# Kernel optimization log

Measured on AMD Instinct MI355X. Metric: run time of the kernel, lower is better.

Reference implementation:

```python
import jax, jax.numpy as jnp
import numpy as np

B, L, C, H = 256, 200, 4, 128


def setup_inputs() -> dict:
    key = jax.random.key(0)
    ks = jax.random.split(key, 6)
    seqs = jax.random.normal(ks[0], (B, L, C, H), dtype=jnp.float32)
    # valid prefix of random length, padding (True) at the tail
    lengths = jax.random.randint(ks[1], (B,), 1, L + 1)
    timeline_mask = (jnp.arange(L)[None, :] >= lengths[:, None])[:, :, None]  # [B,L,1] bool
    attention_mask = jnp.zeros((L, L), dtype=bool)  # unused by the module
    s = 1.0 / np.sqrt(H)  # torch GRU default init U(-1/sqrt(H), 1/sqrt(H))
    W_ih = jax.random.uniform(ks[2], (C, 3 * H, H), minval=-s, maxval=s, dtype=jnp.float32)
    W_hh = jax.random.uniform(ks[3], (C, 3 * H, H), minval=-s, maxval=s, dtype=jnp.float32)
    b_ih = jax.random.uniform(ks[4], (C, 3 * H), minval=-s, maxval=s, dtype=jnp.float32)
    b_hh = jax.random.uniform(ks[5], (C, 3 * H), minval=-s, maxval=s, dtype=jnp.float32)
    return {"seqs": seqs, "timeline_mask": timeline_mask, "attention_mask": attention_mask,
            "W_ih": W_ih, "W_hh": W_hh, "b_ih": b_ih, "b_hh": b_hh}


def batched_roll(x, shifts):
    # x: [B, L, H]; per-sample circular shift along time (torch.roll semantics)
    Ldim = x.shape[1]
    idx = (jnp.arange(Ldim)[None, :] - shifts[:, None]) % Ldim  # [B, L]
    return jnp.take_along_axis(x, idx[:, :, None], axis=1)


def gru(x, W_ih, W_hh, b_ih, b_hh):
    # single-layer batch_first GRU, h0 = 0 (torch nn.GRU math)
    xp = jnp.einsum('blh,gh->blg', x, W_ih) + b_ih  # [B, L, 3H] input projections
    Hd = W_hh.shape[1]

    def step(h, xt):
        gh = h @ W_hh.T + b_hh
        i_r, i_z, i_n = jnp.split(xt, 3, axis=-1)
        h_r, h_z, h_n = jnp.split(gh, 3, axis=-1)
        r = jax.nn.sigmoid(i_r + h_r)
        z = jax.nn.sigmoid(i_z + h_z)
        n = jnp.tanh(i_n + r * h_n)
        h_new = (1.0 - z) * n + z * h
        return h_new, h_new

    h0 = jnp.zeros((x.shape[0], Hd), x.dtype)
    _, ys = jax.lax.scan(step, h0, jnp.swapaxes(xp, 0, 1))  # scan over time
    return jnp.swapaxes(ys, 0, 1)  # [B, L, H]


def reference(seqs, timeline_mask, attention_mask, W_ih, W_hh, b_ih, b_hh):
    mask = timeline_mask[:, :, 0]                 # [B, L] True = pad
    length = jnp.sum(~mask, axis=1)               # count of valid steps
    zero_length = jnp.sum(mask, axis=1)           # count of padded steps
    outs = []
    for i in range(seqs.shape[2]):                # loop over C experts (distinct weights)
        x = batched_roll(seqs[:, :, i, :], length)
        y = gru(x, W_ih[i], W_hh[i], b_ih[i], b_hh[i])
        y = batched_roll(y, zero_length)
        y = jnp.where(timeline_mask, 0.0, y)      # masked_fill(timeline_mask, 0.0)
        outs.append(y)
    return jnp.stack(outs, axis=0)  # [C, B, L, H] (list of experts in the original)
```

## Files before the change

### kernel.cpp

```cpp
#include <hip/hip_runtime.h>
#include <hip/hip_bf16.h>

#define BB 256
#define LL 200
#define CC 4
#define HH 128
#define G3 384
#define XP 136

typedef short bf16x8 __attribute__((ext_vector_type(8)));
typedef float f32x4 __attribute__((ext_vector_type(4)));

#define MFMA16(a, b, c) __builtin_amdgcn_mfma_f32_16x16x32_bf16((a), (b), (c), 0, 0, 0)

__device__ __forceinline__ short bf16_rne(float x) {
    union { float f; unsigned u; } v; v.f = x;
    unsigned r = v.u + 0x7FFFu + ((v.u >> 16) & 1u);
    return (short)(r >> 16);
}
__device__ __forceinline__ float rcp_(float x) { return __builtin_amdgcn_rcpf(x); }
__device__ __forceinline__ float sigm_(float x) { return rcp_(1.0f + __expf(-x)); }
__device__ __forceinline__ float tanhf_(float x) { return 2.0f * rcp_(1.0f + __expf(-2.0f * x)) - 1.0f; }

__device__ __forceinline__ unsigned cvtpk(float lo, float hi) {
    unsigned r;
    asm("v_cvt_pk_bf16_f32 %0, %1, %2" : "=v"(r) : "v"(lo), "v"(hi));
    return r;
}
__device__ __forceinline__ uint2 pack4(float4 v) {
    uint2 p;
    p.x = cvtpk(v.x, v.y);
    p.y = cvtpk(v.z, v.w);
    return p;
}

__global__ void compute_lens_kernel(const unsigned char* __restrict__ mask8,
                                    int* __restrict__ lens) {
    __shared__ int bad;
    int b = threadIdx.x;
    if (b == 0) bad = 0;
    __syncthreads();
    int cnt8 = 0, prev = 0, mono = 1;
    for (int t = 0; t < LL; ++t) {
        int v = mask8[b * LL + t] ? 1 : 0;
        cnt8 += (v == 0);
        if (v < prev) mono = 0;
        prev = v;
    }
    if (!mono) atomicAdd(&bad, 1);
    __syncthreads();
    int len;
    if (bad == 0) {
        len = cnt8;
    } else {
        const int* m32 = (const int*)mask8;
        int c = 0;
        for (int t = 0; t < LL; ++t) c += (m32[b * LL + t] == 0);
        len = c;
    }
    if (len < 1) len = 1;
    if (len > LL) len = LL;
    lens[b] = len;
}

__global__ void wsplit_kernel(const float* __restrict__ Wih, const float* __restrict__ Whh,
                              short* __restrict__ wih_hi, short* __restrict__ whh_hi) {
    int i = blockIdx.x * 256 + threadIdx.x;
    wih_hi[i] = bf16_rne(Wih[i]);
    whh_hi[i] = bf16_rne(Whh[i]);
}

__global__ __launch_bounds__(512, 2) void gru_fused_kernel(
    const float* __restrict__ seqs,
    const int*   __restrict__ lens,
    const short* __restrict__ wih_hi,
    const short* __restrict__ whh_hi,
    const float* __restrict__ b_ih,
    const float* __restrict__ b_hh,
    float*       __restrict__ out)
{
    const int bt = blockIdx.x;
    const int c  = blockIdx.y;
    const int bbase = bt * 16;
    const int tid = threadIdx.x;
    const int w = tid >> 6;
    const int l = tid & 63;
    const int l15 = l & 15, g = l >> 4;

    __shared__ __align__(16) short hA[2][16][XP];
    __shared__ __align__(16) short xs[2][16][XP];

    bf16x8 BH[3][4], WI[3][4];
    #pragma unroll
    for (int q = 0; q < 3; ++q) {
        const int NT = q * 8 + w;
        #pragma unroll
        for (int ks = 0; ks < 4; ++ks) {
            size_t off = (size_t)(c * G3 + NT * 16 + l15) * HH + ks * 32 + g * 8;
            BH[q][ks] = *(const bf16x8*)(whh_hi + off);
            WI[q][ks] = *(const bf16x8*)(wih_hi + off);
        }
    }

    const int dim0 = w * 16 + g * 4;

    f32x4 cR4, cZ4, cHN4, cN4;
    {
        float4 rh = *(const float4*)(b_hh + c * G3 + dim0);
        float4 ri = *(const float4*)(b_ih + c * G3 + dim0);
        float4 zh = *(const float4*)(b_hh + c * G3 + 128 + dim0);
        float4 zi = *(const float4*)(b_ih + c * G3 + 128 + dim0);
        float4 nh = *(const float4*)(b_hh + c * G3 + 256 + dim0);
        float4 ni = *(const float4*)(b_ih + c * G3 + 256 + dim0);
        cR4  = (f32x4){rh.x + ri.x, rh.y + ri.y, rh.z + ri.z, rh.w + ri.w};
        cZ4  = (f32x4){zh.x + zi.x, zh.y + zi.y, zh.z + zi.z, zh.w + zi.w};
        cHN4 = (f32x4){nh.x, nh.y, nh.z, nh.w};
        cN4  = (f32x4){ni.x, ni.y, ni.z, ni.w};
    }
    const f32x4 cZZ = (f32x4){0.f, 0.f, 0.f, 0.f};

    const int bme = bbase + l15;
    const int lenb = lens[bme];
    int tcur = LL - lenb;
    float* optr = out + ((size_t)(c * BB + bme) * LL + tcur) * HH + dim0;
    const ptrdiff_t owrap = (ptrdiff_t)(LL - 1) * HH;
    float hold[4] = { 0.f, 0.f, 0.f, 0.f };

    const int bsl = tid >> 5;
    const int k0s = (tid & 31) * 4;
    const int lenS = lens[bbase + bsl];
    const float* srow0 = seqs + ((size_t)(bbase + bsl) * LL * CC + c) * HH + k0s;
    int ts0 = LL - lenS;
    int ts1 = ts0 + 1; if (ts1 >= LL) ts1 -= LL;
    float4 xr0 = *(const float4*)(srow0 + (size_t)ts0 * (CC * HH));
    float4 xr1 = *(const float4*)(srow0 + (size_t)ts1 * (CC * HH));
    int txs = ts1 + 1; if (txs >= LL) txs -= LL;
    const float* xptr = srow0 + (size_t)txs * (CC * HH);
    const ptrdiff_t xstep = CC * HH;
    const ptrdiff_t xwrap = (ptrdiff_t)(LL - 1) * CC * HH;

    for (int i = tid; i < 16 * XP / 2; i += 512) ((int*)hA[0])[i] = 0;

    *(uint2*)&xs[0][bsl][k0s] = pack4(xr0);
    *(uint2*)&xs[1][bsl][k0s] = pack4(xr1);
    __syncthreads();

    f32x4 xacc[3];
    {
        bf16x8 xb0 = *(const bf16x8*)&xs[0][l15][g * 8];
        xacc[0] = MFMA16(WI[0][0], xb0, cR4);
        xacc[1] = MFMA16(WI[1][0], xb0, cZ4);
        xacc[2] = MFMA16(WI[2][0], xb0, cN4);
        #pragma unroll
        for (int ks = 1; ks < 4; ++ks) {
            bf16x8 xb = *(const bf16x8*)&xs[0][l15][ks * 32 + g * 8];
            #pragma unroll
            for (int q = 0; q < 3; ++q)
                xacc[q] = MFMA16(WI[q][ks], xb, xacc[q]);
        }
    }
    float4 xraw = *(const float4*)xptr;
    txs = (txs + 1 == LL) ? 0 : txs + 1;
    xptr = (txs == 0) ? xptr - xwrap : xptr + xstep;

    __syncthreads();

#define STEP_BODY(HB, HN)                                                      \
    {                                                                          \
        f32x4 racc[3];                                                         \
        {                                                                      \
            bf16x8 hb0 = *(const bf16x8*)&hA[HB][l15][g * 8];                  \
            racc[0] = MFMA16(BH[0][0], hb0, cZZ);                              \
            racc[1] = MFMA16(BH[1][0], hb0, cZZ);                              \
            racc[2] = MFMA16(BH[2][0], hb0, cHN4);                             \
            _Pragma("unroll")                                                  \
            for (int ks = 1; ks < 4; ++ks) {                                   \
                bf16x8 hbf = *(const bf16x8*)&hA[HB][l15][ks * 32 + g * 8];    \
                _Pragma("unroll")                                              \
                for (int q = 0; q < 3; ++q)                                    \
                    racc[q] = MFMA16(BH[q][ks], hbf, racc[q]);                 \
            }                                                                  \
        }                                                                      \
        float hnew[4];                                                         \
        _Pragma("unroll")                                                      \
        for (int r = 0; r < 4; ++r) {                                          \
            float gr = sigm_(racc[0][r] + xacc[0][r]);                         \
            float gz = sigm_(racc[1][r] + xacc[1][r]);                         \
            float gn = tanhf_(xacc[2][r] + gr * racc[2][r]);                   \
            float hv = gn + gz * (hold[r] - gn);                               \
            hnew[r] = hv;                                                      \
            hold[r] = hv;                                                      \
        }                                                                      \
        {                                                                      \
            uint2 pk;                                                          \
            pk.x = cvtpk(hold[0], hold[1]);                                    \
            pk.y = cvtpk(hold[2], hold[3]);                                    \
            *(uint2*)&hA[HN][l15][dim0] = pk;         \
        }                                                                      \
        {                                                                      \
            int valid = tcur < lenb;                                           \
            float4 ov;                                                         \
            ov.x = valid ? hnew[0] : 0.0f;                                     \
            ov.y = valid ? hnew[1] : 0.0f;                                     \
            ov.z = valid ? hnew[2] : 0.0f;                                     \
            ov.w = valid ? hnew[3] : 0.0f;                                     \
            *(float4*)optr = ov;                              \
            int wrapped = (tcur + 1 == LL);                                    \
            tcur = wrapped ? 0 : tcur + 1;                                     \
            optr = wrapped ? optr - owrap : optr + HH;                         \
        }                                                                      \
        {                                                                      \
            bf16x8 xb0 = *(const bf16x8*)&xs[HN][l15][g * 8];                  \
            xacc[0] = MFMA16(WI[0][0], xb0, cR4);                              \
            xacc[1] = MFMA16(WI[1][0], xb0, cZ4);                              \
            xacc[2] = MFMA16(WI[2][0], xb0, cN4);                              \
            _Pragma("unroll")                                                  \
            for (int ks = 1; ks < 4; ++ks) {                                   \
                bf16x8 xb = *(const bf16x8*)&xs[HN][l15][ks * 32 + g * 8];     \
                _Pragma("unroll")                                              \
                for (int q = 0; q < 3; ++q)                                    \
                    xacc[q] = MFMA16(WI[q][ks], xb, xacc[q]);                  \
            }                                                                  \
        }                                                                      \
        *(uint2*)&xs[HB][bsl][k0s] = pack4(xraw);                              \
        xraw = *(const float4*)xptr;                                           \
        txs = (txs + 1 == LL) ? 0 : txs + 1;                                   \
        xptr = (txs == 0) ? xptr - xwrap : xptr + xstep;                       \
        asm volatile("s_waitcnt lgkmcnt(0)" ::: "memory");                     \
        __builtin_amdgcn_s_barrier();                                          \
        __builtin_amdgcn_sched_barrier(0);                                     \
    }

    for (int si2 = 0; si2 < LL; si2 += 2) {
        STEP_BODY(0, 1)
        STEP_BODY(1, 0)
    }
#undef STEP_BODY
}

extern "C" void kernel_launch(void* const* d_in, const int* in_sizes, int n_in,
                              void* d_out, int out_size, void* d_ws, size_t ws_size,
                              hipStream_t stream) {
    const float* seqs  = (const float*)d_in[0];
    const unsigned char* tmask = (const unsigned char*)d_in[1];
    const float* W_ih  = (const float*)d_in[3];
    const float* W_hh  = (const float*)d_in[4];
    const float* b_ih  = (const float*)d_in[5];
    const float* b_hh  = (const float*)d_in[6];
    float* out = (float*)d_out;

    char* ws = (char*)d_ws;
    int*   lens   = (int*)(ws);
    short* wih_hi = (short*)(ws + 1024);
    short* whh_hi = (short*)(ws + 1024 + 393216);

    compute_lens_kernel<<<1, BB, 0, stream>>>(tmask, lens);
    wsplit_kernel<<<768, 256, 0, stream>>>(W_ih, W_hh, wih_hi, whh_hi);

    gru_fused_kernel<<<dim3(16, CC), 512, 0, stream>>>(
        seqs, lens, wih_hi, whh_hi, b_ih, b_hh, out);
}
```

Before: 179.8 us.

## Store h and x staging buffers in MFMA fragment order and halve staging threads

Changes the shared-memory layout of the hidden-state and input staging buffers from padded row-major to a fragment-ordered layout, so each lane reads its bf16x8 MFMA operand with a contiguous, conflict-free 16-byte load. The per-step global loads of the input are now done by 256 threads, each loading 8 floats and writing one 16-byte packed store, instead of 512 threads each handling 4 floats. This targets LDS bank conflicts and address arithmetic in the latency-bound recurrent loop. In exchange, the h writes become scattered stores and the staging work is concentrated in half the threads.

```diff
diff --git a/kernel.cpp b/kernel.cpp
--- a/kernel.cpp
+++ b/kernel.cpp
@@ -6,7 +6,6 @@
 #define CC 4
 #define HH 128
 #define G3 384
-#define XP 136
 
 typedef short bf16x8 __attribute__((ext_vector_type(8)));
 typedef float f32x4 __attribute__((ext_vector_type(4)));
@@ -26,12 +25,6 @@
     unsigned r;
     asm("v_cvt_pk_bf16_f32 %0, %1, %2" : "=v"(r) : "v"(lo), "v"(hi));
     return r;
-}
-__device__ __forceinline__ uint2 pack4(float4 v) {
-    uint2 p;
-    p.x = cvtpk(v.x, v.y);
-    p.y = cvtpk(v.z, v.w);
-    return p;
 }
 
 __global__ void compute_lens_kernel(const unsigned char* __restrict__ mask8,
@@ -87,8 +80,8 @@
     const int l = tid & 63;
     const int l15 = l & 15, g = l >> 4;
 
-    __shared__ __align__(16) short hA[2][16][XP];
-    __shared__ __align__(16) short xs[2][16][XP];
+    __shared__ __align__(16) short hA[2][4][512];
+    __shared__ __align__(16) short xs[2][4][512];
 
     bf16x8 BH[3][4], WI[3][4];
     #pragma unroll
@@ -103,6 +96,8 @@
     }
 
     const int dim0 = w * 16 + g * 4;
+    const int ksw = w >> 1;
+    const int hwbase = ((((w & 1) * 2 + (g >> 1)) * 16 + l15) * 8) + (g & 1) * 4;
 
     f32x4 cR4, cZ4, cHN4, cN4;
     {
@@ -126,56 +121,69 @@
     const ptrdiff_t owrap = (ptrdiff_t)(LL - 1) * HH;
     float hold[4] = { 0.f, 0.f, 0.f, 0.f };
 
-    const int bsl = tid >> 5;
-    const int k0s = (tid & 31) * 4;
-    const int lenS = lens[bbase + bsl];
-    const float* srow0 = seqs + ((size_t)(bbase + bsl) * LL * CC + c) * HH + k0s;
-    int ts0 = LL - lenS;
-    int ts1 = ts0 + 1; if (ts1 >= LL) ts1 -= LL;
-    float4 xr0 = *(const float4*)(srow0 + (size_t)ts0 * (CC * HH));
-    float4 xr1 = *(const float4*)(srow0 + (size_t)ts1 * (CC * HH));
-    int txs = ts1 + 1; if (txs >= LL) txs -= LL;
-    const float* xptr = srow0 + (size_t)txs * (CC * HH);
+    const int sactive = (tid < 256);
+    const int bsl = tid >> 4;
+    const int ko  = (tid & 15) * 8;
+    const int sks = ko >> 5;
+    const int sfb = (((ko >> 3) & 3) * 16 + (bsl & 15)) * 8;
+    const float* srow0 = nullptr;
+    int txs = 0;
+    float4 xra, xrb;
     const ptrdiff_t xstep = CC * HH;
     const ptrdiff_t xwrap = (ptrdiff_t)(LL - 1) * CC * HH;
-
-    for (int i = tid; i < 16 * XP / 2; i += 512) ((int*)hA[0])[i] = 0;
-
-    *(uint2*)&xs[0][bsl][k0s] = pack4(xr0);
-    *(uint2*)&xs[1][bsl][k0s] = pack4(xr1);
+    const float* xptr = nullptr;
+
+    if (sactive) {
+        const int lenS = lens[bbase + bsl];
+        srow0 = seqs + ((size_t)(bbase + bsl) * LL * CC + c) * HH + ko;
+        int ts0 = LL - lenS;
+        int ts1 = ts0 + 1; if (ts1 >= LL) ts1 -= LL;
+        float4 a0 = *(const float4*)(srow0 + (size_t)ts0 * xstep);
+        float4 a1 = *(const float4*)(srow0 + (size_t)ts0 * xstep + 4);
+        float4 b0 = *(const float4*)(srow0 + (size_t)ts1 * xstep);
+        float4 b1 = *(const float4*)(srow0 + (size_t)ts1 * xstep + 4);
+        *(uint4*)&xs[0][sks][sfb] = make_uint4(cvtpk(a0.x, a0.y), cvtpk(a0.z, a0.w),
+                                               cvtpk(a1.x, a1.y), cvtpk(a1.z, a1.w));
+        *(uint4*)&xs[1][sks][sfb] = make_uint4(cvtpk(b0.x, b0.y), cvtpk(b0.z, b0.w),
+                                               cvtpk(b1.x, b1.y), cvtpk(b1.z, b1.w));
+        txs = ts1 + 1; if (txs >= LL) txs -= LL;
+        xptr = srow0 + (size_t)txs * xstep;
+        xra = *(const float4*)xptr;
+        xrb = *(const float4*)(xptr + 4);
+        txs = (txs + 1 == LL) ? 0 : txs + 1;
+        xptr = (txs == 0) ? srow0 : xptr + xstep;
+    }
+
+    for (int i = tid; i < 1024; i += 512) ((int*)hA[0])[i] = 0;
     __syncthreads();
 
     f32x4 xacc[3];
     {
-        bf16x8 xb0 = *(const bf16x8*)&xs[0][l15][g * 8];
+        bf16x8 xb0 = *(const bf16x8*)&xs[0][0][l * 8];
         xacc[0] = MFMA16(WI[0][0], xb0, cR4);
         xacc[1] = MFMA16(WI[1][0], xb0, cZ4);
         xacc[2] = MFMA16(WI[2][0], xb0, cN4);
         #pragma unroll
         for (int ks = 1; ks < 4; ++ks) {
-            bf16x8 xb = *(const bf16x8*)&xs[0][l15][ks * 32 + g * 8];
+            bf16x8 xb = *(const bf16x8*)&xs[0][ks][l * 8];
             #pragma unroll
             for (int q = 0; q < 3; ++q)
                 xacc[q] = MFMA16(WI[q][ks], xb, xacc[q]);
         }
     }
-    float4 xraw = *(const float4*)xptr;
-    txs = (txs + 1 == LL) ? 0 : txs + 1;
-    xptr = (txs == 0) ? xptr - xwrap : xptr + xstep;
-
     __syncthreads();
 
 #define STEP_BODY(HB, HN)                                                      \
     {                                                                          \
         f32x4 racc[3];                                                         \
         {                                                                      \
-            bf16x8 hb0 = *(const bf16x8*)&hA[HB][l15][g * 8];                  \
+            bf16x8 hb0 = *(const bf16x8*)&hA[HB][0][l * 8];                    \
             racc[0] = MFMA16(BH[0][0], hb0, cZZ);                              \
             racc[1] = MFMA16(BH[1][0], hb0, cZZ);                              \
             racc[2] = MFMA16(BH[2][0], hb0, cHN4);                             \
             _Pragma("unroll")                                                  \
             for (int ks = 1; ks < 4; ++ks) {                                   \
-                bf16x8 hbf = *(const bf16x8*)&hA[HB][l15][ks * 32 + g * 8];    \
+                bf16x8 hbf = *(const bf16x8*)&hA[HB][ks][l * 8];               \
                 _Pragma("unroll")                                              \
                 for (int q = 0; q < 3; ++q)                                    \
                     racc[q] = MFMA16(BH[q][ks], hbf, racc[q]);                 \
@@ -195,7 +203,7 @@
             uint2 pk;                                                          \
             pk.x = cvtpk(hold[0], hold[1]);                                    \
             pk.y = cvtpk(hold[2], hold[3]);                                    \
-            *(uint2*)&hA[HN][l15][dim0] = pk;         \
+            *(uint2*)&hA[HN][ksw][hwbase] = pk;       \
         }                                                                      \
         {                                                                      \
             int valid = tcur < lenb;                                           \
@@ -204,28 +212,33 @@
             ov.y = valid ? hnew[1] : 0.0f;                                     \
             ov.z = valid ? hnew[2] : 0.0f;                                     \
             ov.w = valid ? hnew[3] : 0.0f;                                     \
-            *(float4*)optr = ov;                              \
+            *(float4*)optr = ov;                                               \
             int wrapped = (tcur + 1 == LL);                                    \
             tcur = wrapped ? 0 : tcur + 1;                                     \
             optr = wrapped ? optr - owrap : optr + HH;                         \
         }                                                                      \
         {                                                                      \
-            bf16x8 xb0 = *(const bf16x8*)&xs[HN][l15][g * 8];                  \
+            bf16x8 xb0 = *(const bf16x8*)&xs[HN][0][l * 8];                    \
             xacc[0] = MFMA16(WI[0][0], xb0, cR4);                              \
             xacc[1] = MFMA16(WI[1][0], xb0, cZ4);                              \
             xacc[2] = MFMA16(WI[2][0], xb0, cN4);                              \
             _Pragma("unroll")                                                  \
             for (int ks = 1; ks < 4; ++ks) {                                   \
-                bf16x8 xb = *(const bf16x8*)&xs[HN][l15][ks * 32 + g * 8];     \
+                bf16x8 xb = *(const bf16x8*)&xs[HN][ks][l * 8];                \
                 _Pragma("unroll")                                              \
                 for (int q = 0; q < 3; ++q)                                    \
                     xacc[q] = MFMA16(WI[q][ks], xb, xacc[q]);                  \
             }                                                                  \
         }                                                                      \
-        *(uint2*)&xs[HB][bsl][k0s] = pack4(xraw);                              \
-        xraw = *(const float4*)xptr;                                           \
-        txs = (txs + 1 == LL) ? 0 : txs + 1;                                   \
-        xptr = (txs == 0) ? xptr - xwrap : xptr + xstep;                       \
+        if (sactive) {                                                         \
+            *(uint4*)&xs[HB][sks][sfb] = make_uint4(                           \
+                cvtpk(xra.x, xra.y), cvtpk(xra.z, xra.w),                      \
+                cvtpk(xrb.x, xrb.y), cvtpk(xrb.z, xrb.w));                     \
+            xra = *(const float4*)xptr;                                        \
+            xrb = *(const float4*)(xptr + 4);                                  \
+            txs = (txs + 1 == LL) ? 0 : txs + 1;                               \
+            xptr = (txs == 0) ? srow0 : xptr + xstep;                          \
+        }                                                                      \
         asm volatile("s_waitcnt lgkmcnt(0)" ::: "memory");                     \
         __builtin_amdgcn_s_barrier();                                          \
         __builtin_amdgcn_sched_barrier(0);                                     \
```

Measured after the change: 189.4 us. 5.3% more time.
